# Performance work log

Hardware: AMD Instinct MI355X
Metric: run time of the kernel (lower is better)

## Reference

```python
import jax, jax.numpy as jnp
import numpy as np

WINDOW_SIZE = 11
SIGMA = 1.5
C3 = 1e-4
EPS = 1e-12


def _gaussian_window(channels):
    # 1D Gaussian, normalized, then outer product -> 2D separable window
    coords = jnp.arange(WINDOW_SIZE, dtype=jnp.float32) - WINDOW_SIZE // 2
    g = jnp.exp(-coords ** 2 / (2.0 * SIGMA ** 2))
    g = g / g.sum()
    w2 = g[:, None] * g[None, :]                      # [K, K]
    return jnp.broadcast_to(w2, (channels, 1, WINDOW_SIZE, WINDOW_SIZE))


def _dwconv(x, w, channels):
    # depthwise (groups=C) 2D conv with SAME-style symmetric zero padding
    pad = WINDOW_SIZE // 2
    return jax.lax.conv_general_dilated(
        x, w,
        window_strides=(1, 1),
        padding=[(pad, pad), (pad, pad)],
        dimension_numbers=('NCHW', 'OIHW', 'NCHW'),
        feature_group_count=channels,
    )


def reference(x, y):
    x = x.astype(jnp.float32)
    y = y.astype(jnp.float32)
    N, C = x.shape[0], x.shape[1]
    w = _gaussian_window(C)
    mu_x = _dwconv(x, w, C)
    mu_y = _dwconv(y, w, C)
    sigma_xy = _dwconv(x * y, w, C) - mu_x * mu_y
    sigma_x = jnp.clip(_dwconv(x * x, w, C) - mu_x * mu_x, EPS, None)
    sigma_y = jnp.clip(_dwconv(y * y, w, C) - mu_y * mu_y, EPS, None)
    structure = (sigma_xy + C3) / (jnp.sqrt(sigma_x) * jnp.sqrt(sigma_y) + C3)
    structure_mean = structure.reshape(N, C, -1).mean(axis=2)  # [N, C]
    loss = (1.0 - structure_mean).mean()
    return loss


def setup_inputs() -> dict:
    key = jax.random.key(0)
    kx, ky = jax.random.split(key)
    x = jax.random.uniform(kx, (8, 3, 512, 512), dtype=jnp.float32)
    y = jax.random.uniform(ky, (8, 3, 512, 512), dtype=jnp.float32)
    return {"x": x, "y": y}
```

## Files before the change

### kernel.cpp

```cpp
#include <hip/hip_runtime.h>

#define IMG_H 512
#define IMG_W 512
#define NPLANES 24
#define ROWS_PER_BLK 16
#define NITER 26
#define NWAVES 4
#define NBLOCKS (32 * 2 * 24)
#define TOTAL_PIX 6291456.0f

typedef float f32x2 __attribute__((ext_vector_type(2)));

__device__ __constant__ float GW[11] = {
    0.00102838f, 0.00759876f, 0.03600050f, 0.10935817f, 0.21300535f,
    0.26601172f, 0.21300535f, 0.10935817f, 0.03600050f, 0.00759876f,
    0.00102838f};

extern "C" __global__ __launch_bounds__(256) void ssim_structure_kernel(
    const float* __restrict__ x, const float* __restrict__ y,
    float* __restrict__ accum, unsigned int* __restrict__ counter,
    float* __restrict__ out) {
  const int tid = threadIdx.x;
  const int lane = tid & 63;
  const int w = tid >> 6;
  const int band = blockIdx.x;
  const int sgrp = blockIdx.y;
  const int plane = blockIdx.z;

  const size_t pbase = (size_t)plane * IMG_H * IMG_W;
  const float* __restrict__ xp = x + pbase;
  const float* __restrict__ yp = y + pbase;
  const int cbase = (sgrp * NWAVES + w) * 64;
  const int r0 = band * ROWS_PER_BLK;

  __shared__ f32x2 lrow[NWAVES][2][80];

  f32x2 bm[11];
  f32x2 bq[11];
  float bxy[11];

  float acc = 0.0f;

  const int gc = cbase - 5 + lane;
  const int gcc = min(max(gc, 0), IMG_W - 1);
  const float cmask = (gc >= 0 && gc < IMG_W) ? 1.0f : 0.0f;
  const int gc2 = cbase + 59 + lane;
  const int gc2c = min(gc2, IMG_W - 1);
  const float hmask = (gc2 < IMG_W) ? 1.0f : 0.0f;

  f32x2 pre_m = {0.f, 0.f}, pre_e = {0.f, 0.f};

  auto loadrow = [&](int i, f32x2& m, f32x2& e) {
    const int hr = r0 - 5 + i;
    if ((i < NITER) & (hr >= 0) & (hr < IMG_H)) {
      const int rowoff = hr * IMG_W;
      f32x2 v;
      v.x = xp[rowoff + gcc];
      v.y = yp[rowoff + gcc];
      m = v * cmask;
      if (lane < 10) {
        f32x2 h;
        h.x = xp[rowoff + gc2c];
        h.y = yp[rowoff + gc2c];
        e = h * hmask;
      }
    } else {
      m = (f32x2){0.f, 0.f};
      e = (f32x2){0.f, 0.f};
    }
  };

  loadrow(0, pre_m, pre_e);

  for (int ob = 0; ob < 3; ++ob) {
#pragma unroll
    for (int ii = 0; ii < 11; ++ii) {
      const int i = ob * 11 + ii;
      if (i < NITER) {
        const int sel = i & 1;

        lrow[w][sel][lane] = pre_m;
        if (lane < 10) lrow[w][sel][64 + lane] = pre_e;

        loadrow(i + 1, pre_m, pre_e);

        {
          f32x2 tm = {0.f, 0.f};
          f32x2 tq = {0.f, 0.f};
          float txy = 0.f;
#pragma unroll
          for (int d = 0; d < 11; ++d) {
            const f32x2 v = lrow[w][sel][lane + d];
            const float wgt = GW[d];
            const f32x2 wv = v * wgt;
            tm += wv;
            tq = __builtin_elementwise_fma(wv, v, tq);
            txy = fmaf(wv.x, v.y, txy);
          }
          bm[ii] = tm;
          bq[ii] = tq;
          bxy[ii] = txy;
        }

        if (i >= 10) {
          f32x2 vm = {0.f, 0.f};
          f32x2 vq = {0.f, 0.f};
          float vxy = 0.f;
#pragma unroll
          for (int k = 0; k < 11; ++k) {
            const int s = (ii + 1 + k) % 11;
            const float wgt = GW[k];
            const f32x2 w2 = {wgt, wgt};
            vm = __builtin_elementwise_fma(bm[s], w2, vm);
            vq = __builtin_elementwise_fma(bq[s], w2, vq);
            vxy = fmaf(wgt, bxy[s], vxy);
          }
          const float sxy = fmaf(-vm.x, vm.y, vxy);
          f32x2 sp = __builtin_elementwise_fma(-vm, vm, vq);
          sp = __builtin_elementwise_max(sp, (f32x2){1e-12f, 1e-12f});
          const float denom = sqrtf(sp.x) * sqrtf(sp.y) + 1e-4f;
          acc += (sxy + 1e-4f) / denom;
        }
      }
    }
  }

#pragma unroll
  for (int off = 32; off > 0; off >>= 1) acc += __shfl_down(acc, off, 64);
  __shared__ float wsum[NWAVES];
  if (lane == 0) wsum[w] = acc;
  __syncthreads();
  if (tid == 0) {
    float bsum = 0.f;
#pragma unroll
    for (int v = 0; v < NWAVES; ++v) bsum += wsum[v];
    atomicAdd(accum, bsum);
    __threadfence();
    const unsigned int ret = atomicAdd(counter, 1u);
    if (ret == (unsigned int)(NBLOCKS - 1)) {
      __threadfence();
      const float total = atomicAdd(accum, 0.0f);
      out[0] = 1.0f - total * (1.0f / TOTAL_PIX);
    }
  }
}

extern "C" void kernel_launch(void* const* d_in, const int* in_sizes, int n_in,
                              void* d_out, int out_size, void* d_ws,
                              size_t ws_size, hipStream_t stream) {
  const float* x = (const float*)d_in[0];
  const float* y = (const float*)d_in[1];
  float* out = (float*)d_out;
  float* accum = (float*)d_ws;
  unsigned int* counter = (unsigned int*)((char*)d_ws + sizeof(float));

  hipMemsetAsync(d_ws, 0, 2 * sizeof(float), stream);

  dim3 grid(IMG_H / ROWS_PER_BLK, 2, NPLANES);
  ssim_structure_kernel<<<grid, 256, 0, stream>>>(x, y, accum, counter, out);
}
```

Measured before the change: 147.2 us.

## Vectorize row loads, deepen prefetch, use 512-thread blocks and fast reciprocal

Each block now has 8 waves covering a full 512-column row, so the 2-way column split of the grid goes away. Loads are now float2 vectors from 38 lanes, stored interleaved into LDS as float4, which replaces the scalar loads plus halo loads. Prefetch depth grows to three rows, the Gaussian weights become compile-time constants, the loop is fully unrolled, and the division plus two square roots become one sqrt and rcp. This raises register pressure and lowers occupancy granularity, and the approximate rcp adds a small precision risk.

```diff
diff --git a/kernel.cpp b/kernel.cpp
--- a/kernel.cpp
+++ b/kernel.cpp
@@ -5,18 +5,18 @@
 #define NPLANES 24
 #define ROWS_PER_BLK 16
 #define NITER 26
-#define NWAVES 4
-#define NBLOCKS (32 * 2 * 24)
+#define NBLOCKS (32 * 24)
 #define TOTAL_PIX 6291456.0f
 
 typedef float f32x2 __attribute__((ext_vector_type(2)));
+typedef float f32x4 __attribute__((ext_vector_type(4)));
 
-__device__ __constant__ float GW[11] = {
+constexpr float GWc[11] = {
     0.00102838f, 0.00759876f, 0.03600050f, 0.10935817f, 0.21300535f,
     0.26601172f, 0.21300535f, 0.10935817f, 0.03600050f, 0.00759876f,
     0.00102838f};
 
-extern "C" __global__ __launch_bounds__(256) void ssim_structure_kernel(
+extern "C" __global__ __launch_bounds__(512) void ssim_structure_kernel(
     const float* __restrict__ x, const float* __restrict__ y,
     float* __restrict__ accum, unsigned int* __restrict__ counter,
     float* __restrict__ out) {
@@ -24,116 +24,110 @@
   const int lane = tid & 63;
   const int w = tid >> 6;
   const int band = blockIdx.x;
-  const int sgrp = blockIdx.y;
-  const int plane = blockIdx.z;
+  const int plane = blockIdx.y;
 
   const size_t pbase = (size_t)plane * IMG_H * IMG_W;
   const float* __restrict__ xp = x + pbase;
   const float* __restrict__ yp = y + pbase;
-  const int cbase = (sgrp * NWAVES + w) * 64;
   const int r0 = band * ROWS_PER_BLK;
+  const int cbase = w * 64;
 
-  __shared__ f32x2 lrow[NWAVES][2][80];
+  __shared__ __align__(16) f32x2 lrow[8][2][80];
 
   f32x2 bm[11];
   f32x2 bq[11];
   float bxy[11];
 
+  const int c0 = cbase - 6 + 2 * lane;
+  const bool ld_active = (lane < 38);
+  const int cc = min(max(c0, 0), IMG_W - 2);
+  const float m0 = (c0 >= 0 && c0 < IMG_W) ? 1.f : 0.f;
+  const float m1 = (c0 + 1 >= 0 && c0 + 1 < IMG_W) ? 1.f : 0.f;
+  const f32x2 mask = {m0, m1};
+
+  f32x2 px[3], py[3];
+
   float acc = 0.0f;
 
-  const int gc = cbase - 5 + lane;
-  const int gcc = min(max(gc, 0), IMG_W - 1);
-  const float cmask = (gc >= 0 && gc < IMG_W) ? 1.0f : 0.0f;
-  const int gc2 = cbase + 59 + lane;
-  const int gc2c = min(gc2, IMG_W - 1);
-  const float hmask = (gc2 < IMG_W) ? 1.0f : 0.0f;
-
-  f32x2 pre_m = {0.f, 0.f}, pre_e = {0.f, 0.f};
-
-  auto loadrow = [&](int i, f32x2& m, f32x2& e) {
+  auto loadrow = [&](int i, f32x2& vx, f32x2& vy) {
     const int hr = r0 - 5 + i;
-    if ((i < NITER) & (hr >= 0) & (hr < IMG_H)) {
-      const int rowoff = hr * IMG_W;
-      f32x2 v;
-      v.x = xp[rowoff + gcc];
-      v.y = yp[rowoff + gcc];
-      m = v * cmask;
-      if (lane < 10) {
-        f32x2 h;
-        h.x = xp[rowoff + gc2c];
-        h.y = yp[rowoff + gc2c];
-        e = h * hmask;
-      }
+    if ((i < NITER) && (hr >= 0) && (hr < IMG_H) && ld_active) {
+      const int off = hr * IMG_W + cc;
+      vx = *reinterpret_cast<const f32x2*>(xp + off);
+      vy = *reinterpret_cast<const f32x2*>(yp + off);
     } else {
-      m = (f32x2){0.f, 0.f};
-      e = (f32x2){0.f, 0.f};
+      vx = (f32x2){0.f, 0.f};
+      vy = (f32x2){0.f, 0.f};
     }
   };
 
-  loadrow(0, pre_m, pre_e);
+  loadrow(0, px[0], py[0]);
+  loadrow(1, px[1], py[1]);
+  loadrow(2, px[2], py[2]);
 
-  for (int ob = 0; ob < 3; ++ob) {
 #pragma unroll
-    for (int ii = 0; ii < 11; ++ii) {
-      const int i = ob * 11 + ii;
-      if (i < NITER) {
-        const int sel = i & 1;
+  for (int i = 0; i < NITER; ++i) {
+    const int s = i % 3;
+    const int sel = i & 1;
+    const int ii = i % 11;
 
-        lrow[w][sel][lane] = pre_m;
-        if (lane < 10) lrow[w][sel][64 + lane] = pre_e;
+    if (ld_active) {
+      const f32x2 mx = px[s] * mask;
+      const f32x2 my = py[s] * mask;
+      const f32x4 st = {mx.x, my.x, mx.y, my.y};
+      *reinterpret_cast<f32x4*>(&lrow[w][sel][2 * lane]) = st;
+    }
 
-        loadrow(i + 1, pre_m, pre_e);
+    loadrow(i + 3, px[s], py[s]);
 
-        {
-          f32x2 tm = {0.f, 0.f};
-          f32x2 tq = {0.f, 0.f};
-          float txy = 0.f;
+    {
+      f32x2 tm = {0.f, 0.f};
+      f32x2 tq = {0.f, 0.f};
+      float txy = 0.f;
 #pragma unroll
-          for (int d = 0; d < 11; ++d) {
-            const f32x2 v = lrow[w][sel][lane + d];
-            const float wgt = GW[d];
-            const f32x2 wv = v * wgt;
-            tm += wv;
-            tq = __builtin_elementwise_fma(wv, v, tq);
-            txy = fmaf(wv.x, v.y, txy);
-          }
-          bm[ii] = tm;
-          bq[ii] = tq;
-          bxy[ii] = txy;
-        }
+      for (int d = 0; d < 11; ++d) {
+        const f32x2 v = lrow[w][sel][lane + 1 + d];
+        const float wgt = GWc[d];
+        const f32x2 wv = v * wgt;
+        tm += wv;
+        tq = __builtin_elementwise_fma(wv, v, tq);
+        txy = fmaf(wv.x, v.y, txy);
+      }
+      bm[ii] = tm;
+      bq[ii] = tq;
+      bxy[ii] = txy;
+    }
 
-        if (i >= 10) {
-          f32x2 vm = {0.f, 0.f};
-          f32x2 vq = {0.f, 0.f};
-          float vxy = 0.f;
+    if (i >= 10) {
+      f32x2 vm = {0.f, 0.f};
+      f32x2 vq = {0.f, 0.f};
+      float vxy = 0.f;
 #pragma unroll
-          for (int k = 0; k < 11; ++k) {
-            const int s = (ii + 1 + k) % 11;
-            const float wgt = GW[k];
-            const f32x2 w2 = {wgt, wgt};
-            vm = __builtin_elementwise_fma(bm[s], w2, vm);
-            vq = __builtin_elementwise_fma(bq[s], w2, vq);
-            vxy = fmaf(wgt, bxy[s], vxy);
-          }
-          const float sxy = fmaf(-vm.x, vm.y, vxy);
-          f32x2 sp = __builtin_elementwise_fma(-vm, vm, vq);
-          sp = __builtin_elementwise_max(sp, (f32x2){1e-12f, 1e-12f});
-          const float denom = sqrtf(sp.x) * sqrtf(sp.y) + 1e-4f;
-          acc += (sxy + 1e-4f) / denom;
-        }
+      for (int k = 0; k < 11; ++k) {
+        const int s2 = (ii + 1 + k) % 11;
+        const float wgt = GWc[k];
+        const f32x2 w2 = {wgt, wgt};
+        vm = __builtin_elementwise_fma(bm[s2], w2, vm);
+        vq = __builtin_elementwise_fma(bq[s2], w2, vq);
+        vxy = fmaf(wgt, bxy[s2], vxy);
       }
+      const float sxy = fmaf(-vm.x, vm.y, vxy);
+      f32x2 sp = __builtin_elementwise_fma(-vm, vm, vq);
+      sp = __builtin_elementwise_max(sp, (f32x2){1e-12f, 1e-12f});
+      const float den = sqrtf(sp.x * sp.y) + 1e-4f;
+      acc = fmaf(sxy + 1e-4f, __builtin_amdgcn_rcpf(den), acc);
     }
   }
 
 #pragma unroll
   for (int off = 32; off > 0; off >>= 1) acc += __shfl_down(acc, off, 64);
-  __shared__ float wsum[NWAVES];
+  __shared__ float wsum[8];
   if (lane == 0) wsum[w] = acc;
   __syncthreads();
   if (tid == 0) {
     float bsum = 0.f;
 #pragma unroll
-    for (int v = 0; v < NWAVES; ++v) bsum += wsum[v];
+    for (int v = 0; v < 8; ++v) bsum += wsum[v];
     atomicAdd(accum, bsum);
     __threadfence();
     const unsigned int ret = atomicAdd(counter, 1u);
@@ -156,6 +150,6 @@
 
   hipMemsetAsync(d_ws, 0, 2 * sizeof(float), stream);
 
-  dim3 grid(IMG_H / ROWS_PER_BLK, 2, NPLANES);
-  ssim_structure_kernel<<<grid, 256, 0, stream>>>(x, y, accum, counter, out);
+  dim3 grid(IMG_H / ROWS_PER_BLK, NPLANES);
+  ssim_structure_kernel<<<grid, 512, 0, stream>>>(x, y, accum, counter, out);
 }
```

Result: slower. 342.3 us (+132.5%).
